# Kernel tuning notes

Hardware: AMD Instinct MI355X
Metric: run time of the kernel (lower is better)

## Reference

```python
import jax, jax.numpy as jnp
import numpy as np

B, N, D = 2, 2048, 1024
H, HD = 16, 64
BASE = 10000.0
INIT_STD = 0.02


def apply_rope(x, base=BASE):
    """Rotary embedding on the last dim; seq axis is axis 1.

    Works for q of shape (b, n, h, d) and k of shape (b, n, d).
    """
    d = x.shape[-1]
    n = x.shape[1]
    half = d // 2
    inv_freq = 1.0 / (base ** (jnp.arange(half, dtype=jnp.float32) / half))
    ang = jnp.arange(n, dtype=jnp.float32)[:, None] * inv_freq  # (n, d/2)
    extra = x.ndim - 3  # axes between seq axis and feature axis
    ang = ang.reshape((n,) + (1,) * extra + (half,))
    cos, sin = jnp.cos(ang), jnp.sin(ang)
    x1, x2 = jnp.split(x, 2, axis=-1)
    return jnp.concatenate([x1 * cos - x2 * sin, x2 * cos + x1 * sin], axis=-1)


def setup_inputs() -> dict:
    key = jax.random.key(0)
    kx, k1, k2, k3, k4 = jax.random.split(key, 5)
    x = jax.random.normal(kx, (B, N, D), dtype=jnp.float32)
    Wq = jax.random.normal(k1, (D, H * HD), dtype=jnp.float32) * INIT_STD
    Wkv = jax.random.normal(k2, (D, 2 * HD), dtype=jnp.float32) * INIT_STD
    Wkvh = jax.random.normal(k3, (D, 2 * H), dtype=jnp.float32) * INIT_STD
    Wo = jax.random.normal(k4, (H * HD, D), dtype=jnp.float32) * INIT_STD
    return {"x": x, "Wq": Wq, "Wkv": Wkv, "Wkvh": Wkvh, "Wo": Wo}


def reference(x, Wq, Wkv, Wkvh, Wo):
    b, n, d = x.shape
    q = (x @ Wq).reshape(b, n, H, HD)          # (b,n,h,hd)
    kv = x @ Wkv                                # (b,n,2*hd)
    kv_head = jax.nn.sigmoid(x @ Wkvh)          # (b,n,2*h)
    k, v = jnp.split(kv, 2, axis=-1)            # each (b,n,hd)
    k_head, v_head = jnp.split(kv_head, 2, axis=-1)  # each (b,n,h)

    # LRPE (rotary) on q and on the shared low-rank k
    q = apply_rope(q)
    k = apply_rope(k)

    # outer-product expansion: (b,n,h) x (b,n,hd) -> (b,n,h,hd)
    k = jnp.einsum('bnh,bnd->bnhd', k_head, k)
    v = jnp.einsum('bnh,bnd->bnhd', v_head, v)

    # causal softmax attention, scale = 1/sqrt(head_dim)
    scale = 1.0 / np.sqrt(HD)
    scores = jnp.einsum('bqhd,bkhd->bhqk', q, k) * scale
    mask = jnp.tril(jnp.ones((n, n), dtype=bool))
    scores = jnp.where(mask, scores, jnp.finfo(scores.dtype).min)
    p = jax.nn.softmax(scores, axis=-1)
    out = jnp.einsum('bhqk,bkhd->bqhd', p, v)   # (b,n,h,hd)

    out = out.reshape(b, n, H * HD)
    return out @ Wo
```

## Files before the change

kernel.cpp:

```cpp
#include <hip/hip_runtime.h>

typedef unsigned short u16;
typedef unsigned int u32;
typedef __attribute__((ext_vector_type(8))) short short8;
typedef __attribute__((ext_vector_type(4))) float f32x4;
typedef __attribute__((ext_vector_type(4))) u32 u32x4;
typedef __attribute__((ext_vector_type(2))) u32 u32x2;
typedef __attribute__((ext_vector_type(4))) u16 u16x4;

#define AS1 __attribute__((address_space(1)))
#define AS3 __attribute__((address_space(3)))

constexpr int B_ = 2, N_ = 2048, H_ = 16;
constexpr int ROWS = B_ * N_;
constexpr float LOG2E = 1.44269504088896f;

__device__ __forceinline__ float bf2f(u16 u){ union{u32 u; float f;} v; v.u = ((u32)u)<<16; return v.f; }
__device__ __forceinline__ u16 f2bf(float f){
  union{float f; u32 u;} v; v.f = f;
  u32 u = v.u; u += 0x7fffu + ((u>>16)&1u);
  return (u16)(u>>16);
}
__device__ __forceinline__ u32 cvtpk(float lo, float hi){
  u32 r; asm("v_cvt_pk_bf16_f32 %0, %1, %2" : "=v"(r) : "v"(lo), "v"(hi)); return r;
}

__global__ __launch_bounds__(256) void k_setup(const float* __restrict__ x, u16* __restrict__ xb,
                                               float2* __restrict__ tab,
                                               const float* __restrict__ Wq, const float* __restrict__ Wo,
                                               u16* __restrict__ WqT, u16* __restrict__ WoT,
                                               const float* __restrict__ Wkv, const float* __restrict__ Wkvh,
                                               u16* __restrict__ WkvT){
  __shared__ float T[64*65];
  int bid = blockIdx.x, tid = threadIdx.x;
  if (bid < 4096){
    int i = (bid*256 + tid)*4;
    f32x4 v = *(const f32x4*)(x + i);
    u16x4 o; o[0]=f2bf(v[0]); o[1]=f2bf(v[1]); o[2]=f2bf(v[2]); o[3]=f2bf(v[3]);
    *(u16x4*)(xb + i) = o;
    return;
  }
  if (bid < 4352){
    int idx = (bid-4096)*256 + tid;
    int i = idx & 31, n = idx >> 5;
    float ang = (float)n * exp2f(-(float)i * 0.4152410118609203f);
    tab[idx] = make_float2(cosf(ang), sinf(ang));
    return;
  }
  if (bid < 4864){
    int m = (bid - 4352) >> 8;
    const float* in = m ? Wo : Wq;
    u16* out = m ? WoT : WqT;
    int t2 = (bid - 4352) & 255;
    int n0 = (t2 & 15) << 6, k0 = (t2 >> 4) << 6;
    #pragma unroll
    for (int s=0; s<4; ++s){
      int chunk = tid + s*256, r = chunk >> 4, c4 = (chunk & 15) << 2;
      *(f32x4*)(&T[r*65 + c4]) = *(const f32x4*)(&in[(size_t)(k0 + r)*1024 + n0 + c4]);
    }
    __syncthreads();
    #pragma unroll
    for (int s=0; s<2; ++s){
      int chunk = tid + s*256, d = chunk >> 3, c8 = (chunk & 7) << 3;
      u16x4 o1, o2;
      #pragma unroll
      for (int j=0; j<4; ++j){ o1[j] = f2bf(T[(c8+j)*65 + d]); o2[j] = f2bf(T[(c8+4+j)*65 + d]); }
      *(u16x4*)(&out[(size_t)(n0 + d)*1024 + k0 + c8])     = o1;
      *(u16x4*)(&out[(size_t)(n0 + d)*1024 + k0 + c8 + 4]) = o2;
    }
    return;
  }
  {
    int idx = (bid - 4864)*256 + tid;
    int n = idx >> 10, k = idx & 1023;
    float v = 0.f;
    if (n < 128)      v = Wkv[k*128 + n];
    else if (n < 160) v = Wkvh[k*32 + (n-128)];
    WkvT[idx] = f2bf(v);
  }
}

template<int MODE>
__global__ __launch_bounds__(256) void k_gemm_mn(const u16* __restrict__ A, const u16* __restrict__ Bt,
                                                 void* __restrict__ Cv, float* __restrict__ proj,
                                                 const float2* __restrict__ tab,
                                                 int M, int N, int K){
  __shared__ u16 As[128*64];
  __shared__ u16 Bs[64*64];
  int ntile = N >> 6;
  int m0 = (blockIdx.x / ntile) << 7;
  int n0 = (blockIdx.x % ntile) << 6;
  int tid = threadIdx.x;
  int l = tid & 63, lr = l & 15, lc = l >> 4;
  int w = tid >> 6;
  int wm = w * 32;
  f32x4 acc[2][4] = {};
  for (int kt = 0; kt < K; kt += 64){
    __syncthreads();
    #pragma unroll
    for (int s = 0; s < 4; ++s){
      int chunk = tid + s*256, r = chunk >> 3, c8 = (chunk & 7) << 3;
      __builtin_amdgcn_global_load_lds(
        (const AS1 u32*)(&A[(size_t)(m0 + r)*K + kt + c8]),
        (AS3 u32*)(&As[r*64 + c8]), 16, 0, 0);
    }
    #pragma unroll
    for (int s = 0; s < 2; ++s){
      int chunk = tid + s*256, r = chunk >> 3, c8 = (chunk & 7) << 3;
      __builtin_amdgcn_global_load_lds(
        (const AS1 u32*)(&Bt[(size_t)(n0 + r)*K + kt + c8]),
        (AS3 u32*)(&Bs[r*64 + c8]), 16, 0, 0);
    }
    __syncthreads();
    short8 af[2][2], bfr[4][2];
    #pragma unroll
    for (int m=0; m<2; ++m)
      #pragma unroll
      for (int c=0; c<2; ++c)
        af[m][c] = *(const short8*)(&As[(wm + m*16 + lr)*64 + c*32 + lc*8]);
    #pragma unroll
    for (int n=0; n<4; ++n)
      #pragma unroll
      for (int c=0; c<2; ++c)
        bfr[n][c] = *(const short8*)(&Bs[(n*16 + lr)*64 + c*32 + lc*8]);
    __builtin_amdgcn_s_setprio(1);
    #pragma unroll
    for (int m=0; m<2; ++m)
      #pragma unroll
      for (int n=0; n<4; ++n)
        #pragma unroll
        for (int c=0; c<2; ++c)
          acc[m][n] = __builtin_amdgcn_mfma_f32_16x16x32_bf16(af[m][c], bfr[n][c], acc[m][n], 0,0,0);
    __builtin_amdgcn_s_setprio(0);
  }
  if constexpr (MODE == 0){
    float* C = (float*)Cv;
    #pragma unroll
    for (int m=0; m<2; ++m)
      #pragma unroll
      for (int n=0; n<4; ++n)
        #pragma unroll
        for (int r=0; r<4; ++r)
          C[(size_t)(m0 + wm + m*16 + lc*4 + r)*N + n0 + n*16 + lr] = acc[m][n][r];
  } else {
    if (n0 < 1024){
      u16* C = (u16*)Cv;
      #pragma unroll
      for (int m=0; m<2; ++m){
        int grow = m0 + wm + m*16 + lc*4;
        #pragma unroll
        for (int nf=0; nf<2; ++nf){
          int i = nf*16 + lr;
          #pragma unroll
          for (int r=0; r<4; ++r){
            float2 cs = tab[(size_t)((grow + r) & (N_-1))*32 + i];
            float x1 = acc[m][nf][r], x2 = acc[m][nf+2][r];
            C[(size_t)(grow + r)*1024 + n0 + i]      = f2bf(0.125f*(x1*cs.x - x2*cs.y));
            C[(size_t)(grow + r)*1024 + n0 + i + 32] = f2bf(0.125f*(x2*cs.x + x1*cs.y));
          }
        }
      }
    } else {
      int pc = n0 - 1024;
      #pragma unroll
      for (int m=0; m<2; ++m)
        #pragma unroll
        for (int n=0; n<4; ++n)
          #pragma unroll
          for (int r=0; r<4; ++r)
            proj[(size_t)(m0 + wm + m*16 + lc*4 + r)*192 + pc + n*16 + lr] = acc[m][n][r];
    }
  }
}

__global__ __launch_bounds__(256) void k_postproc2(const float* __restrict__ proj, const float2* __restrict__ tab,
                                                   u16* __restrict__ k_rope, float* __restrict__ k_head,
                                                   float* __restrict__ v_head, u16* __restrict__ vt){
  __shared__ u16 Tv[64*72];
  int n0 = blockIdx.x << 6;
  int b = n0 >> 11;
  int tid = threadIdx.x;
  #pragma unroll
  for (int s=0; s<4; ++s){
    int chunk = tid + s*256, r = chunk >> 4, c4 = (chunk & 15) << 2;
    f32x4 v = *(const f32x4*)(&proj[(size_t)(n0+r)*192 + 64 + c4]);
    u16x4 o; o[0]=f2bf(v[0]); o[1]=f2bf(v[1]); o[2]=f2bf(v[2]); o[3]=f2bf(v[3]);
    *(u16x4*)(&Tv[r*72 + c4]) = o;
  }
  int wv = tid>>6, t = tid&63;
  for (int rr = wv; rr < 64; rr += 4){
    int row = n0 + rr, n = row & (N_-1);
    const float* p = proj + (size_t)row*192;
    if (t < 32){
      float hv = 1.f/(1.f + __expf(-p[128 + t]));
      if (t < 16) k_head[((size_t)b*16 + t)*N_ + n] = hv * LOG2E;
      else        v_head[((size_t)b*16 + (t-16))*N_ + n] = hv;
      float2 cs = tab[n*32 + t];
      float k1 = p[t], k2 = p[32 + t];
      k_rope[(size_t)row*64 + t]      = f2bf(k1*cs.x - k2*cs.y);
      k_rope[(size_t)row*64 + 32 + t] = f2bf(k2*cs.x + k1*cs.y);
    }
  }
  __syncthreads();
  int nb = n0 & (N_-1);
  #pragma unroll
  for (int s=0; s<2; ++s){
    int chunk = tid + s*256, d = chunk>>3, c8 = (chunk&7)<<3;
    u32x4 o; u16* op = (u16*)&o;
    #pragma unroll
    for (int j=0; j<8; ++j) op[j] = Tv[(c8+j)*72 + d];
    *(u32x4*)(&vt[((size_t)b*64 + d)*N_ + nb + c8]) = o;
  }
}

__global__ __launch_bounds__(256, 4) void k_attn13(const u16* __restrict__ q_bf, const u16* __restrict__ k_rp,
                                                   const u16* __restrict__ vt, const float* __restrict__ k_hd,
                                                   const float* __restrict__ v_hd,
                                                   u16* __restrict__ o_part, float* __restrict__ l_part){
  __shared__ u16 Ks[64*72];
  __shared__ u16 Vts[64*72];
  __shared__ float g_s[128];
  int z = blockIdx.x;
  int pidx = (int)((u32)z / 3u);
  int sp = z - pidx*3;
  int qt = 31 - (pidx >> 5);
  int h = pidx & 15, b = (pidx >> 4) & 1;
  int nt = qt + 1;
  int t0 = (sp*nt)/3, t1 = ((sp+1)*nt)/3;
  int tid = threadIdx.x, w = tid>>6, l = tid&63, lr = l&15, lc = l>>4;
  if (t0 >= t1){
    u16* op = o_part + (size_t)z*4096;
    for (int i = tid; i < 512; i += 256) *(u32x4*)(op + i*8) = (u32x4){0,0,0,0};
    if (tid < 64) l_part[z*64 + tid] = 0.f;
    return;
  }
  size_t rowbase = (size_t)b*N_;
  size_t qoff = (rowbase + qt*64 + w*16 + lr)*1024 + h*64;
  short8 qf0 = *(const short8*)(&q_bf[qoff + lc*8]);
  short8 qf1 = *(const short8*)(&q_bf[qoff + 32 + lc*8]);
  const float* gkp = k_hd + ((size_t)b*16 + h)*N_;
  const float* gvp = v_hd + ((size_t)b*16 + h)*N_;
  u32x4 kr[2], vr[2]; float gr;
  auto issue = [&](int t){
    int kg0 = t << 6;
    #pragma unroll
    for (int s=0; s<2; ++s){
      int chunk = tid + s*256, r = chunk>>3, c8 = (chunk&7)<<3;
      kr[s] = *(const u32x4*)(&k_rp[(rowbase + kg0 + r)*64 + c8]);
      vr[s] = *(const u32x4*)(&vt[((size_t)b*64 + r)*N_ + kg0 + c8]);
    }
    gr = (tid < 64) ? gkp[kg0 + tid] : ((tid < 128) ? gvp[kg0 + tid - 64] : 0.f);
  };
  float lsum = 0.f;
  f32x4 o[4] = {};
  issue(t0);
  for (int t = t0; t < t1; ++t){
    int kg0 = t << 6;
    __syncthreads();
    #pragma unroll
    for (int s=0; s<2; ++s){
      int chunk = tid + s*256, r = chunk>>3, c8 = (chunk&7)<<3;
      *(u32x4*)(&Ks[r*72 + c8]) = kr[s];
      {
        int wbase = (c8 >> 5) << 5;
        int cp = (c8 & 31) >> 3;
        int g0 = (cp & 1)*16 + (cp >> 1)*4;
        u32x2 lov = { vr[s][0], vr[s][1] };
        u32x2 hiv = { vr[s][2], vr[s][3] };
        *(u32x2*)(&Vts[r*72 + wbase + g0])     = lov;
        *(u32x2*)(&Vts[r*72 + wbase + g0 + 8]) = hiv;
      }
    }
    if (tid < 128) g_s[tid] = gr;
    if (t + 1 < t1) issue(t+1);
    __syncthreads();
    f32x4 s4[4];
    __builtin_amdgcn_s_setprio(1);
    #pragma unroll
    for (int nf=0; nf<4; ++nf){
      short8 kf0 = *(const short8*)(&Ks[(nf*16+lr)*72 + lc*8]);
      short8 kf1 = *(const short8*)(&Ks[(nf*16+lr)*72 + 32 + lc*8]);
      f32x4 zz = {};
      zz = __builtin_amdgcn_mfma_f32_16x16x32_bf16(kf0, qf0, zz, 0,0,0);
      s4[nf] = __builtin_amdgcn_mfma_f32_16x16x32_bf16(kf1, qf1, zz, 0,0,0);
    }
    __builtin_amdgcn_s_setprio(0);
    #pragma unroll
    for (int nf=0; nf<4; ++nf){
      f32x4 gkv = *(const f32x4*)(&g_s[nf*16 + lc*4]);
      #pragma unroll
      for (int r=0; r<4; ++r) s4[nf][r] *= gkv[r];
    }
    if (t == qt){
      int qg = qt*64 + w*16 + lr;
      #pragma unroll
      for (int nf=0; nf<4; ++nf)
        #pragma unroll
        for (int r=0; r<4; ++r)
          if (kg0 + nf*16 + lc*4 + r > qg) s4[nf][r] = -1e30f;
    }
    #pragma unroll
    for (int nf=0; nf<4; ++nf)
      #pragma unroll
      for (int r=0; r<4; ++r){ s4[nf][r] = exp2f(s4[nf][r]); lsum += s4[nf][r]; }
    u32 w0[4], w1[4];
    #pragma unroll
    for (int nf=0; nf<4; ++nf){
      f32x4 gvv = *(const f32x4*)(&g_s[64 + nf*16 + lc*4]);
      w0[nf] = cvtpk(s4[nf][0]*gvv[0], s4[nf][1]*gvv[1]);
      w1[nf] = cvtpk(s4[nf][2]*gvv[2], s4[nf][3]*gvv[3]);
    }
    union PF { u32x4 u; short8 s; } pf0, pf1;
    pf0.u = (u32x4){ w0[0], w1[0], w0[1], w1[1] };
    pf1.u = (u32x4){ w0[2], w1[2], w0[3], w1[3] };
    __builtin_amdgcn_s_setprio(1);
    #pragma unroll
    for (int nf=0; nf<4; ++nf){
      short8 vf0 = *(const short8*)(&Vts[(nf*16+lr)*72 + lc*8]);
      short8 vf1 = *(const short8*)(&Vts[(nf*16+lr)*72 + 32 + lc*8]);
      o[nf] = __builtin_amdgcn_mfma_f32_16x16x32_bf16(pf0.s, vf0, o[nf], 0,0,0);
      o[nf] = __builtin_amdgcn_mfma_f32_16x16x32_bf16(pf1.s, vf1, o[nf], 0,0,0);
    }
    __builtin_amdgcn_s_setprio(0);
  }
  lsum += __shfl_xor(lsum, 16);
  lsum += __shfl_xor(lsum, 32);
  if (lc == 0) l_part[z*64 + w*16 + lr] = lsum;
  u16* op = o_part + (size_t)z*4096;
  #pragma unroll
  for (int nf=0; nf<4; ++nf)
    #pragma unroll
    for (int r=0; r<4; ++r)
      op[(w*16 + lc*4 + r)*64 + nf*16 + lr] = f2bf(o[nf][r]);
}

__global__ __launch_bounds__(256) void k_comb(const u16* __restrict__ o_part, const float* __restrict__ l_part,
                                              u16* __restrict__ attn_o){
  int z2 = blockIdx.x;
  int qt = 31 - (z2 >> 5), h = z2 & 15, b = (z2 >> 4) & 1;
  int tid = threadIdx.x;
  int q = tid >> 2, c16 = (tid & 3) << 4;
  size_t base0 = (size_t)(3*z2)*4096 + q*64 + c16;
  float lv = l_part[(3*z2)*64 + q] + l_part[(3*z2+1)*64 + q] + l_part[(3*z2+2)*64 + q];
  float rl = __builtin_amdgcn_rcpf(lv);
  union U8 { u32x4 v; u16 s[8]; };
  U8 a0, a1, b0, b1, c0, c1, r0, r1;
  a0.v = *(const u32x4*)(o_part + base0);
  a1.v = *(const u32x4*)(o_part + base0 + 8);
  b0.v = *(const u32x4*)(o_part + base0 + 4096);
  b1.v = *(const u32x4*)(o_part + base0 + 4096 + 8);
  c0.v = *(const u32x4*)(o_part + base0 + 8192);
  c1.v = *(const u32x4*)(o_part + base0 + 8192 + 8);
  #pragma unroll
  for (int j=0; j<8; ++j){
    r0.s[j] = f2bf((bf2f(a0.s[j]) + bf2f(b0.s[j]) + bf2f(c0.s[j])) * rl);
    r1.s[j] = f2bf((bf2f(a1.s[j]) + bf2f(b1.s[j]) + bf2f(c1.s[j])) * rl);
  }
  u16* outp = attn_o + ((size_t)(b*N_ + qt*64 + q))*1024 + h*64 + c16;
  *(u32x4*)outp = r0.v;
  *(u32x4*)(outp + 8) = r1.v;
}

extern "C" void kernel_launch(void* const* d_in, const int* in_sizes, int n_in,
                              void* d_out, int out_size, void* d_ws, size_t ws_size,
                              hipStream_t stream){
  const float* x    = (const float*)d_in[0];
  const float* Wq   = (const float*)d_in[1];
  const float* Wkv  = (const float*)d_in[2];
  const float* Wkvh = (const float*)d_in[3];
  const float* Wo   = (const float*)d_in[4];
  float* out = (float*)d_out;

  char* p = (char*)d_ws;
  u16* xb      = (u16*)p;   p += (size_t)ROWS*1024*2;
  u16* WT      = (u16*)p;   p += (size_t)1216*1024*2;
  u16* WoT     = (u16*)p;   p += (size_t)1024*1024*2;
  float* proj  = (float*)p; p += (size_t)ROWS*192*4;
  u16* q_bf    = (u16*)p;   p += (size_t)ROWS*1024*2;
  u16* k_rp    = (u16*)p;   p += (size_t)ROWS*64*2;
  u16* vt      = (u16*)p;   p += (size_t)B_*64*N_*2;
  float* k_hd  = (float*)p; p += (size_t)B_*H_*N_*4;
  float* v_hd  = (float*)p; p += (size_t)B_*H_*N_*4;
  float2* tab  = (float2*)p; p += (size_t)N_*32*8;
  u16* o_part  = (u16*)p;   p += (size_t)3072*4096*2;
  float* l_part= (float*)p; p += (size_t)3072*64*4;
  u16* attn_o  = xb;

  k_setup<<<4096 + 256 + 512 + 768, 256, 0, stream>>>(x, xb, tab, Wq, Wo, WT, WoT,
                                                      Wkv, Wkvh, WT + (size_t)1024*1024);
  k_gemm_mn<1><<<(ROWS/128)*(1216/64), 256, 0, stream>>>(xb, WT, q_bf, proj, tab, ROWS, 1216, 1024);
  k_postproc2<<<ROWS/64, 256, 0, stream>>>(proj, tab, k_rp, k_hd, v_hd, vt);
  k_attn13<<<3072, 256, 0, stream>>>(q_bf, k_rp, vt, k_hd, v_hd, o_part, l_part);
  k_comb<<<1024, 256, 0, stream>>>(o_part, l_part, attn_o);
  k_gemm_mn<0><<<(ROWS/128)*(1024/64), 256, 0, stream>>>(attn_o, WoT, out, nullptr, nullptr, ROWS, 1024, 1024);
}
```

Measured before the change: 109.4 us.

## Shrink GEMM tiles to 64x64 and transpose Wkv/Wkvh via LDS tiles

Both projection GEMMs now use 64x64 output tiles instead of 128x64, doubling the block count to improve occupancy and load balance across CUs at the cost of lower data reuse per tile. Each wave now computes a 16x64 slice. The Wkv/Wkvh transpose in the setup kernel moves from one scalar element per thread with strided reads to 48 blocks that stage 64x64 tiles through shared memory, using coalesced vector loads and stores. This cuts the setup grid from 768 to 48 blocks for that part.

```diff
diff --git a/kernel.cpp b/kernel.cpp
--- a/kernel.cpp
+++ b/kernel.cpp
@@ -71,53 +71,64 @@
     return;
   }
   {
-    int idx = (bid - 4864)*256 + tid;
-    int n = idx >> 10, k = idx & 1023;
-    float v = 0.f;
-    if (n < 128)      v = Wkv[k*128 + n];
-    else if (n < 160) v = Wkvh[k*32 + (n-128)];
-    WkvT[idx] = f2bf(v);
+    int bid2 = bid - 4864;
+    int kt = (bid2 < 32) ? (bid2 >> 1) : (bid2 - 32);
+    int k0 = kt << 6;
+    int nout0 = (bid2 < 32) ? ((bid2 & 1) << 6) : 128;
+    bool is_kvh = (bid2 >= 32);
+    #pragma unroll
+    for (int s=0; s<4; ++s){
+      int chunk = tid + s*256, r = chunk >> 4, c4 = (chunk & 15) << 2;
+      f32x4 v = {0.f,0.f,0.f,0.f};
+      if (!is_kvh) v = *(const f32x4*)(&Wkv[(size_t)(k0 + r)*128 + nout0 + c4]);
+      else if (c4 < 32) v = *(const f32x4*)(&Wkvh[(size_t)(k0 + r)*32 + c4]);
+      *(f32x4*)(&T[r*65 + c4]) = v;
+    }
+    __syncthreads();
+    #pragma unroll
+    for (int s=0; s<2; ++s){
+      int chunk = tid + s*256, d = chunk >> 3, c8 = (chunk & 7) << 3;
+      u16x4 o1, o2;
+      #pragma unroll
+      for (int j=0; j<4; ++j){ o1[j] = f2bf(T[(c8+j)*65 + d]); o2[j] = f2bf(T[(c8+4+j)*65 + d]); }
+      *(u16x4*)(&WkvT[(size_t)(nout0 + d)*1024 + k0 + c8])     = o1;
+      *(u16x4*)(&WkvT[(size_t)(nout0 + d)*1024 + k0 + c8 + 4]) = o2;
+    }
   }
 }
 
 template<int MODE>
-__global__ __launch_bounds__(256) void k_gemm_mn(const u16* __restrict__ A, const u16* __restrict__ Bt,
-                                                 void* __restrict__ Cv, float* __restrict__ proj,
-                                                 const float2* __restrict__ tab,
-                                                 int M, int N, int K){
-  __shared__ u16 As[128*64];
+__global__ __launch_bounds__(256) void k_gemm64(const u16* __restrict__ A, const u16* __restrict__ Bt,
+                                                void* __restrict__ Cv, float* __restrict__ proj,
+                                                const float2* __restrict__ tab,
+                                                int M, int N, int K){
+  __shared__ u16 As[64*64];
   __shared__ u16 Bs[64*64];
   int ntile = N >> 6;
-  int m0 = (blockIdx.x / ntile) << 7;
+  int m0 = (blockIdx.x / ntile) << 6;
   int n0 = (blockIdx.x % ntile) << 6;
   int tid = threadIdx.x;
   int l = tid & 63, lr = l & 15, lc = l >> 4;
   int w = tid >> 6;
-  int wm = w * 32;
-  f32x4 acc[2][4] = {};
+  int wm = w * 16;
+  f32x4 acc[4] = {};
   for (int kt = 0; kt < K; kt += 64){
     __syncthreads();
     #pragma unroll
-    for (int s = 0; s < 4; ++s){
+    for (int s = 0; s < 2; ++s){
       int chunk = tid + s*256, r = chunk >> 3, c8 = (chunk & 7) << 3;
       __builtin_amdgcn_global_load_lds(
         (const AS1 u32*)(&A[(size_t)(m0 + r)*K + kt + c8]),
         (AS3 u32*)(&As[r*64 + c8]), 16, 0, 0);
-    }
-    #pragma unroll
-    for (int s = 0; s < 2; ++s){
-      int chunk = tid + s*256, r = chunk >> 3, c8 = (chunk & 7) << 3;
       __builtin_amdgcn_global_load_lds(
         (const AS1 u32*)(&Bt[(size_t)(n0 + r)*K + kt + c8]),
         (AS3 u32*)(&Bs[r*64 + c8]), 16, 0, 0);
     }
     __syncthreads();
-    short8 af[2][2], bfr[4][2];
-    #pragma unroll
-    for (int m=0; m<2; ++m)
-      #pragma unroll
-      for (int c=0; c<2; ++c)
-        af[m][c] = *(const short8*)(&As[(wm + m*16 + lr)*64 + c*32 + lc*8]);
+    short8 af[2], bfr[4][2];
+    #pragma unroll
+    for (int c=0; c<2; ++c)
+      af[c] = *(const short8*)(&As[(wm + lr)*64 + c*32 + lc*8]);
     #pragma unroll
     for (int n=0; n<4; ++n)
       #pragma unroll
@@ -125,50 +136,41 @@
         bfr[n][c] = *(const short8*)(&Bs[(n*16 + lr)*64 + c*32 + lc*8]);
     __builtin_amdgcn_s_setprio(1);
     #pragma unroll
-    for (int m=0; m<2; ++m)
-      #pragma unroll
-      for (int n=0; n<4; ++n)
-        #pragma unroll
-        for (int c=0; c<2; ++c)
-          acc[m][n] = __builtin_amdgcn_mfma_f32_16x16x32_bf16(af[m][c], bfr[n][c], acc[m][n], 0,0,0);
+    for (int n=0; n<4; ++n)
+      #pragma unroll
+      for (int c=0; c<2; ++c)
+        acc[n] = __builtin_amdgcn_mfma_f32_16x16x32_bf16(af[c], bfr[n][c], acc[n], 0,0,0);
     __builtin_amdgcn_s_setprio(0);
   }
   if constexpr (MODE == 0){
     float* C = (float*)Cv;
     #pragma unroll
-    for (int m=0; m<2; ++m)
-      #pragma unroll
-      for (int n=0; n<4; ++n)
-        #pragma unroll
-        for (int r=0; r<4; ++r)
-          C[(size_t)(m0 + wm + m*16 + lc*4 + r)*N + n0 + n*16 + lr] = acc[m][n][r];
+    for (int n=0; n<4; ++n)
+      #pragma unroll
+      for (int r=0; r<4; ++r)
+        C[(size_t)(m0 + wm + lc*4 + r)*N + n0 + n*16 + lr] = acc[n][r];
   } else {
     if (n0 < 1024){
       u16* C = (u16*)Cv;
-      #pragma unroll
-      for (int m=0; m<2; ++m){
-        int grow = m0 + wm + m*16 + lc*4;
+      int grow = m0 + wm + lc*4;
+      #pragma unroll
+      for (int nf=0; nf<2; ++nf){
+        int i = nf*16 + lr;
         #pragma unroll
-        for (int nf=0; nf<2; ++nf){
-          int i = nf*16 + lr;
-          #pragma unroll
-          for (int r=0; r<4; ++r){
-            float2 cs = tab[(size_t)((grow + r) & (N_-1))*32 + i];
-            float x1 = acc[m][nf][r], x2 = acc[m][nf+2][r];
-            C[(size_t)(grow + r)*1024 + n0 + i]      = f2bf(0.125f*(x1*cs.x - x2*cs.y));
-            C[(size_t)(grow + r)*1024 + n0 + i + 32] = f2bf(0.125f*(x2*cs.x + x1*cs.y));
-          }
+        for (int r=0; r<4; ++r){
+          float2 cs = tab[(size_t)((grow + r) & (N_-1))*32 + i];
+          float x1 = acc[nf][r], x2 = acc[nf+2][r];
+          C[(size_t)(grow + r)*1024 + n0 + i]      = f2bf(0.125f*(x1*cs.x - x2*cs.y));
+          C[(size_t)(grow + r)*1024 + n0 + i + 32] = f2bf(0.125f*(x2*cs.x + x1*cs.y));
         }
       }
     } else {
       int pc = n0 - 1024;
       #pragma unroll
-      for (int m=0; m<2; ++m)
+      for (int n=0; n<4; ++n)
         #pragma unroll
-        for (int n=0; n<4; ++n)
-          #pragma unroll
-          for (int r=0; r<4; ++r)
-            proj[(size_t)(m0 + wm + m*16 + lc*4 + r)*192 + pc + n*16 + lr] = acc[m][n][r];
+        for (int r=0; r<4; ++r)
+          proj[(size_t)(m0 + wm + lc*4 + r)*192 + pc + n*16 + lr] = acc[n][r];
     }
   }
 }
@@ -386,11 +388,11 @@
   float* l_part= (float*)p; p += (size_t)3072*64*4;
   u16* attn_o  = xb;
 
-  k_setup<<<4096 + 256 + 512 + 768, 256, 0, stream>>>(x, xb, tab, Wq, Wo, WT, WoT,
-                                                      Wkv, Wkvh, WT + (size_t)1024*1024);
-  k_gemm_mn<1><<<(ROWS/128)*(1216/64), 256, 0, stream>>>(xb, WT, q_bf, proj, tab, ROWS, 1216, 1024);
+  k_setup<<<4096 + 256 + 512 + 48, 256, 0, stream>>>(x, xb, tab, Wq, Wo, WT, WoT,
+                                                     Wkv, Wkvh, WT + (size_t)1024*1024);
+  k_gemm64<1><<<(ROWS/64)*(1216/64), 256, 0, stream>>>(xb, WT, q_bf, proj, tab, ROWS, 1216, 1024);
   k_postproc2<<<ROWS/64, 256, 0, stream>>>(proj, tab, k_rp, k_hd, v_hd, vt);
   k_attn13<<<3072, 256, 0, stream>>>(q_bf, k_rp, vt, k_hd, v_hd, o_part, l_part);
   k_comb<<<1024, 256, 0, stream>>>(o_part, l_part, attn_o);
-  k_gemm_mn<0><<<(ROWS/128)*(1024/64), 256, 0, stream>>>(attn_o, WoT, out, nullptr, nullptr, ROWS, 1024, 1024);
-}
+  k_gemm64<0><<<(ROWS/64)*(1024/64), 256, 0, stream>>>(attn_o, WoT, out, nullptr, nullptr, ROWS, 1024, 1024);
+}
```

Result: slower. 122.3 us (+11.9%).
